# Kernel tuning notes

Hardware: AMD Instinct MI355X
Metric: run time of the kernel (lower is better)

The kernel has to match this reference:

```python
import jax, jax.numpy as jnp
import numpy as np

B, S, D = 32, 512, 512
H, DK, DV, DFF = 8, 64, 64, 2048
TEMP = float(np.sqrt(DK))  # d_k ** 0.5
COS_EPS = 1e-8             # torch.cosine_similarity eps
LN_EPS = 1e-5


def _layernorm(x, g, b):
    mu = jnp.mean(x, axis=-1, keepdims=True)
    var = jnp.var(x, axis=-1, keepdims=True)
    return (x - mu) * jax.lax.rsqrt(var + LN_EPS) * g + b


def setup_inputs() -> dict:
    key = jax.random.key(0)
    ks = jax.random.split(key, 12)
    s = 0.02
    return {
        "x": jax.random.normal(ks[0], (B, S, D), dtype=jnp.float32),
        "w_q": jax.random.normal(ks[1], (D, H * DK), dtype=jnp.float32) * s,
        "w_k": jax.random.normal(ks[2], (D, H * DK), dtype=jnp.float32) * s,
        "w_v": jax.random.normal(ks[3], (D, H * DV), dtype=jnp.float32) * s,
        "w_o": jax.random.normal(ks[4], (H * DV, D), dtype=jnp.float32) * s,
        "w_ff1": jax.random.normal(ks[5], (D, DFF), dtype=jnp.float32) * s,
        "b_ff1": jnp.zeros((DFF,), dtype=jnp.float32),
        "w_ff2": jax.random.normal(ks[6], (DFF, D), dtype=jnp.float32) * s,
        "b_ff2": jnp.zeros((D,), dtype=jnp.float32),
        "g1": jnp.ones((D,), dtype=jnp.float32),
        "b1": jnp.zeros((D,), dtype=jnp.float32),
        "g2": jnp.ones((D,), dtype=jnp.float32),
        "b2": jnp.zeros((D,), dtype=jnp.float32),
    }


def reference(x, w_q, w_k, w_v, w_o, w_ff1, b_ff1, w_ff2, b_ff2, g1, b1, g2, b2):
    b, s, _ = x.shape
    # projections -> [b, h, s, d]
    q = (x @ w_q).reshape(b, s, H, DK).transpose(0, 2, 1, 3)
    k = (x @ w_k).reshape(b, s, H, DK).transpose(0, 2, 1, 3)
    v = (x @ w_v).reshape(b, s, H, DV).transpose(0, 2, 1, 3)
    # cosine-similarity attention: dot(q,k) / max(||q||*||k||, eps) / temperature
    scores = jnp.einsum("bhqd,bhkd->bhqk", q, k)
    nq = jnp.linalg.norm(q, axis=-1)  # [b,h,s]
    nk = jnp.linalg.norm(k, axis=-1)
    denom = jnp.maximum(nq[:, :, :, None] * nk[:, :, None, :], COS_EPS)
    attn = jax.nn.softmax(scores / denom / TEMP, axis=-1)
    out = jnp.einsum("bhqk,bhkd->bhqd", attn, v)  # [b,h,s,dv]
    out = out.transpose(0, 2, 1, 3).reshape(b, s, H * DV) @ w_o
    # residual + LN1
    h1 = _layernorm(x + out, g1, b1)
    # FFN
    ffn = jax.nn.relu(h1 @ w_ff1 + b_ff1) @ w_ff2 + b_ff2
    # residual + LN2
    return _layernorm(h1 + ffn, g2, b2)
```

## Files before the change

### kernel.cpp

```cpp
#include <hip/hip_runtime.h>
#include <cmath>

typedef __bf16 bf16x8 __attribute__((ext_vector_type(8)));
typedef __bf16 bf16x4 __attribute__((ext_vector_type(4)));
typedef float  floatx4 __attribute__((ext_vector_type(4)));

#define LN_EPS 1e-5f
#define INV_TEMP 0.125f

static const int Mrows = 16384;

__device__ __forceinline__ void gload_lds16(const void* g, void* l) {
  __builtin_amdgcn_global_load_lds(
      (const __attribute__((address_space(1))) void*)g,
      (__attribute__((address_space(3))) void*)l, 16, 0, 0);
}

__global__ __launch_bounds__(256) void prep_kernel(const float* __restrict__ x, __bf16* __restrict__ xb,
                                                   const float* __restrict__ wq, const float* __restrict__ wk,
                                                   const float* __restrict__ wv, const float* __restrict__ wo,
                                                   const float* __restrict__ wff1, const float* __restrict__ wff2,
                                                   __bf16* __restrict__ tq, __bf16* __restrict__ tk,
                                                   __bf16* __restrict__ tv, __bf16* __restrict__ to_,
                                                   __bf16* __restrict__ tff1, __bf16* __restrict__ tff2) {
  const int bid = blockIdx.x, tid = threadIdx.x;
  if (bid < 8192) {
    int i = bid * 256 + tid;
    float4 v = ((const float4*)x)[i];
    __bf16* d = xb + i * 4;
    d[0] = (__bf16)v.x; d[1] = (__bf16)v.y; d[2] = (__bf16)v.z; d[3] = (__bf16)v.w;
    return;
  }
  __shared__ __bf16 til[64][72];
  int t = bid - 8192;
  const float* src; __bf16* dst; int R, C, bx, by;
  if (t < 256) {
    int w = t >> 6, tt = t & 63;
    const float* srcs[4] = {wq, wk, wv, wo};
    __bf16* dsts[4] = {tq, tk, tv, to_};
    src = srcs[w]; dst = dsts[w]; R = 512; C = 512; bx = tt & 7; by = tt >> 3;
  } else if (t < 512) {
    int tt = t - 256;
    src = wff1; dst = tff1; R = 512; C = 2048; bx = tt & 31; by = tt >> 5;
  } else {
    int tt = t - 512;
    src = wff2; dst = tff2; R = 2048; C = 512; bx = tt & 7; by = tt >> 3;
  }
  const float* s = src + (size_t)(by * 64) * C + bx * 64;
  int r = tid >> 4, c4 = (tid & 15) * 4;
  for (int p = 0; p < 4; ++p) {
    int rr = r + p * 16;
    float4 v = *(const float4*)(s + (size_t)rr * C + c4);
    til[c4 + 0][rr] = (__bf16)v.x;
    til[c4 + 1][rr] = (__bf16)v.y;
    til[c4 + 2][rr] = (__bf16)v.z;
    til[c4 + 3][rr] = (__bf16)v.w;
  }
  __syncthreads();
  __bf16* d = dst + (size_t)(bx * 64) * R + by * 64;
  int orow = tid >> 3, oc8 = (tid & 7) * 8;
  for (int p = 0; p < 2; ++p) {
    int rr = orow + p * 32;
    *(bf16x8*)(d + (size_t)rr * R + oc8) = *(const bf16x8*)(&til[rr][oc8]);
  }
}

template <int EPI, int NBN, int NDIM, int KDIM>
__global__ __launch_bounds__(256) void gemm_bt(const __bf16* __restrict__ A,
                                               const __bf16* __restrict__ Bt,
                                               __bf16* __restrict__ Cv,
                                               const float* __restrict__ bias,
                                               float* __restrict__ norms,
                                               __bf16* __restrict__ vtg) {
  __shared__ __align__(16) char smem[128 * 144 * 2];
  __bf16* As = (__bf16*)smem;
  __bf16* Bs = (__bf16*)(smem + 16384);
  const int tid = threadIdx.x;
  const int wave = tid >> 6, lane = tid & 63;
  const int l15 = lane & 15, quad = lane >> 4;
  const int id = blockIdx.x;
  const int xcd = id & 7, t = id >> 3;
  const int nblk = t % NBN, mblk = (t / NBN) * 8 + xcd;
  const int m0 = mblk * 128, n0 = nblk * 128;
  const int wrow = (wave >> 1) * 64, wcol = (wave & 1) * 64;
  const int rs = lane >> 3;
  const int swz_st = ((lane & 7) ^ rs) * 8;
  const int s7 = l15 & 7;

  floatx4 zero = {0.f, 0.f, 0.f, 0.f};
  floatx4 acc[4][4];
  for (int i = 0; i < 4; ++i)
    for (int j = 0; j < 4; ++j) acc[i][j] = zero;

  for (int kt = 0; kt < KDIM; kt += 64) {
    __syncthreads();
    for (int c = 0; c < 8; ++c) {
      int g = wave * 8 + c;
      const __bf16* src;
      __bf16* dst;
      if (g < 16) {
        int row = m0 + g * 8 + rs;
        src = A + (size_t)row * KDIM + kt + swz_st;
        dst = As + g * 512;
      } else {
        int g2 = g - 16;
        int row = n0 + g2 * 8 + rs;
        src = Bt + (size_t)row * KDIM + kt + swz_st;
        dst = Bs + g2 * 512;
      }
      gload_lds16(src, dst + lane * 8);
    }
    __syncthreads();
    for (int hh = 0; hh < 2; ++hh) {
      int ko = ((hh * 4 + quad) ^ s7) * 8;
      bf16x8 a[4], b[4];
      for (int i = 0; i < 4; ++i)
        a[i] = *(const bf16x8*)(As + (wrow + i * 16 + l15) * 64 + ko);
      for (int j = 0; j < 4; ++j)
        b[j] = *(const bf16x8*)(Bs + (wcol + j * 16 + l15) * 64 + ko);
      for (int i = 0; i < 4; ++i)
        for (int j = 0; j < 4; ++j)
          acc[i][j] = __builtin_amdgcn_mfma_f32_16x16x32_bf16(a[i], b[j], acc[i][j], 0, 0, 0);
    }
  }

  if (EPI == 4) {
    int head_global = (n0 + wcol) >> 6;
    int kind = head_global >> 3;
    if (kind < 2) {
      int h = head_global & 7;
      for (int i = 0; i < 4; ++i)
        for (int r = 0; r < 4; ++r) {
          float sq = 0.f;
          for (int j = 0; j < 4; ++j) {
            float v = acc[i][j][r];
            sq += v * v;
          }
          for (int m = 1; m < 16; m <<= 1) sq += __shfl_xor(sq, m, 64);
          if (l15 == 0) {
            int arow = m0 + wrow + i * 16 + quad * 4 + r;
            int bb = arow >> 9, ss = arow & 511;
            norms[kind * 131072 + ((bb << 3) + h) * 512 + ss] = rsqrtf(sq);
          }
        }
    } else {
      __syncthreads();
      __bf16* Ct = (__bf16*)smem;
      for (int i = 0; i < 4; ++i)
        for (int j = 0; j < 4; ++j) {
          bf16x4 pk;
          for (int r = 0; r < 4; ++r) pk[r] = (__bf16)acc[i][j][r];
          *(bf16x4*)(Ct + (wcol + j * 16 + l15) * 136 + wrow + i * 16 + quad * 4) = pk;
        }
      __syncthreads();
      int b = mblk >> 2, s0r = (mblk & 3) * 128;
      for (int p = 0; p < 8; ++p) {
        int row = p * 16 + (tid >> 4);
        int c8 = (tid & 15) * 8;
        int colg = n0 + row;
        int h = (colg >> 6) & 7, d = colg & 63;
        *(bf16x8*)(vtg + ((size_t)(((b << 3) + h) * 64 + d)) * 512 + s0r + c8) =
            *(const bf16x8*)(Ct + row * 136 + c8);
      }
      return;
    }
  }

  __syncthreads();
  __bf16* Cs = (__bf16*)smem;
  for (int i = 0; i < 4; ++i)
    for (int j = 0; j < 4; ++j) {
      int coll = wcol + j * 16 + l15;
      float bv = (EPI == 2) ? bias[n0 + coll] : 0.f;
      for (int r = 0; r < 4; ++r) {
        float v = acc[i][j][r];
        if (EPI == 2) {
          v += bv;
          v = v > 0.f ? v : 0.f;
        }
        Cs[(wrow + i * 16 + quad * 4 + r) * 144 + coll] = (__bf16)v;
      }
    }
  __syncthreads();
  for (int p = 0; p < 8; ++p) {
    int row = p * 16 + (tid >> 4);
    int c8 = (tid & 15) * 8;
    *(bf16x8*)(Cv + (size_t)(m0 + row) * NDIM + n0 + c8) =
        *(const bf16x8*)(Cs + row * 144 + c8);
  }
}

__global__ __launch_bounds__(256) void attn_kernel(const __bf16* __restrict__ qkv,
                                                   const __bf16* __restrict__ vtg,
                                                   const float* __restrict__ norms,
                                                   __bf16* __restrict__ out) {
  __shared__ __align__(16) __bf16 Ks[64 * 64];
  __shared__ __align__(16) __bf16 Vs[64 * 64];
  __shared__ __align__(16) __bf16 P2[4][16 * 72];
  const int tid = threadIdx.x, wave = tid >> 6, lane = tid & 63;
  const int l15 = lane & 15, quad = lane >> 4;
  const int bh = blockIdx.x & 255;
  const int qq = blockIdx.x >> 8;
  const int b = bh >> 3, h = bh & 7;
  const int qbase = qq * 128 + wave * 32;
  const int rs = lane >> 3;
  const int swz_st = ((lane & 7) ^ rs) * 8;
  const int s7 = l15 & 7;

  const __bf16* Qb = qkv + (size_t)(b * 512) * 1536 + h * 64;
  const __bf16* Kb = Qb + 512;
  const __bf16* Vtb = vtg + (size_t)bh * 32768;
  const float* nkinv = norms + 131072 + bh * 512;
  const float* nqinv = norms + bh * 512;
  __bf16* Pw = P2[wave];

  bf16x8 aq[2][2];
  float cq[2];
  for (int ch = 0; ch < 2; ++ch) {
    int qrow = qbase + ch * 16;
    aq[ch][0] = *(const bf16x8*)(Qb + (size_t)(qrow + l15) * 1536 + quad * 8);
    aq[ch][1] = *(const bf16x8*)(Qb + (size_t)(qrow + l15) * 1536 + 32 + quad * 8);
    cq[ch] = nqinv[qrow + l15] * INV_TEMP;
  }

  floatx4 zero = {0.f, 0.f, 0.f, 0.f};
  floatx4 o[2][4];
  float lsum[2] = {0.f, 0.f};
  for (int ch = 0; ch < 2; ++ch)
    for (int jd = 0; jd < 4; ++jd) o[ch][jd] = zero;

  for (int kt = 0; kt < 8; ++kt) {
    int s0 = kt * 64;
    __syncthreads();
    for (int c = 0; c < 4; ++c) {
      int g = wave * 4 + c;
      const __bf16* src;
      __bf16* dst;
      if (g < 8) {
        int sk = g * 8 + rs;
        src = Kb + (size_t)(s0 + sk) * 1536 + swz_st;
        dst = Ks + g * 512;
      } else {
        int g2 = g - 8;
        int d = g2 * 8 + rs;
        src = Vtb + (size_t)d * 512 + s0 + swz_st;
        dst = Vs + g2 * 512;
      }
      gload_lds16(src, dst + lane * 8);
    }
    __syncthreads();

    for (int ch = 0; ch < 2; ++ch) {
      floatx4 z[4];
      for (int j = 0; j < 4; ++j) {
        int r64 = (j * 16 + l15) * 64;
        bf16x8 k0 = *(const bf16x8*)(Ks + r64 + ((quad ^ s7) * 8));
        bf16x8 k1 = *(const bf16x8*)(Ks + r64 + (((4 + quad) ^ s7) * 8));
        floatx4 zz = zero;
        zz = __builtin_amdgcn_mfma_f32_16x16x32_bf16(k0, aq[ch][0], zz, 0, 0, 0);
        zz = __builtin_amdgcn_mfma_f32_16x16x32_bf16(k1, aq[ch][1], zz, 0, 0, 0);
        z[j] = zz;
      }
      for (int j = 0; j < 4; ++j) {
        floatx4 nk4 = *(const floatx4*)(nkinv + s0 + j * 16 + quad * 4);
        bf16x4 pk;
        for (int r = 0; r < 4; ++r) {
          float p = __expf(z[j][r] * cq[ch] * nk4[r]);
          lsum[ch] += p;
          pk[r] = (__bf16)p;
        }
        *(bf16x4*)(Pw + l15 * 72 + j * 16 + quad * 4) = pk;
      }
      bf16x8 ap0 = *(const bf16x8*)(Pw + l15 * 72 + quad * 8);
      bf16x8 ap1 = *(const bf16x8*)(Pw + l15 * 72 + 32 + quad * 8);
      for (int jd = 0; jd < 4; ++jd) {
        int r64 = (jd * 16 + l15) * 64;
        bf16x8 v0 = *(const bf16x8*)(Vs + r64 + ((quad ^ s7) * 8));
        bf16x8 v1 = *(const bf16x8*)(Vs + r64 + (((4 + quad) ^ s7) * 8));
        o[ch][jd] = __builtin_amdgcn_mfma_f32_16x16x32_bf16(v0, ap0, o[ch][jd], 0, 0, 0);
        o[ch][jd] = __builtin_amdgcn_mfma_f32_16x16x32_bf16(v1, ap1, o[ch][jd], 0, 0, 0);
      }
    }
  }

  for (int ch = 0; ch < 2; ++ch) {
    float s = lsum[ch];
    s += __shfl_xor(s, 16, 64);
    s += __shfl_xor(s, 32, 64);
    float inv = __builtin_amdgcn_rcpf(s);
    int q = qbase + ch * 16 + l15;
    __bf16* op = out + (size_t)(b * 512 + q) * 512 + h * 64;
    for (int jd = 0; jd < 4; ++jd) {
      bf16x4 pk;
      for (int r = 0; r < 4; ++r) pk[r] = (__bf16)(o[ch][jd][r] * inv);
      *(bf16x4*)(op + jd * 16 + quad * 4) = pk;
    }
  }
}

template <bool X1BF, bool WF, bool WB>
__global__ __launch_bounds__(256) void resid_ln(const float* __restrict__ X1f,
                                                const __bf16* __restrict__ X1b,
                                                const __bf16* __restrict__ X2,
                                                const float* __restrict__ bias,
                                                const float* __restrict__ g,
                                                const float* __restrict__ be,
                                                float* __restrict__ outf,
                                                __bf16* __restrict__ outb) {
  int row = blockIdx.x * 4 + (threadIdx.x >> 6);
  int lane = threadIdx.x & 63;
  float v[8];
  bf16x8 b8 = *(const bf16x8*)(X2 + (size_t)row * 512 + lane * 8);
  if (X1BF) {
    bf16x8 a = *(const bf16x8*)(X1b + (size_t)row * 512 + lane * 8);
    for (int i = 0; i < 8; ++i) v[i] = (float)a[i] + (float)b8[i];
  } else {
    const float4* r1 = (const float4*)(X1f + (size_t)row * 512);
    float4 a0 = r1[lane * 2], a1 = r1[lane * 2 + 1];
    v[0] = a0.x; v[1] = a0.y; v[2] = a0.z; v[3] = a0.w;
    v[4] = a1.x; v[5] = a1.y; v[6] = a1.z; v[7] = a1.w;
    for (int i = 0; i < 8; ++i) v[i] += (float)b8[i];
  }
  if (bias) {
    const float* bp = bias + lane * 8;
    for (int i = 0; i < 8; ++i) v[i] += bp[i];
  }
  float s = 0.f, sq = 0.f;
  for (int i = 0; i < 8; ++i) {
    s += v[i];
    sq += v[i] * v[i];
  }
  for (int m = 1; m < 64; m <<= 1) {
    s += __shfl_xor(s, m, 64);
    sq += __shfl_xor(sq, m, 64);
  }
  float mean = s * (1.f / 512.f);
  float var = sq * (1.f / 512.f) - mean * mean;
  float rstd = rsqrtf(var + LN_EPS);
  const float* gp = g + lane * 8;
  const float* bp2 = be + lane * 8;
  float o[8];
  for (int i = 0; i < 8; ++i) o[i] = (v[i] - mean) * rstd * gp[i] + bp2[i];
  if (WF) {
    float4 w0 = {o[0], o[1], o[2], o[3]}, w1 = {o[4], o[5], o[6], o[7]};
    ((float4*)(outf + (size_t)row * 512))[lane * 2] = w0;
    ((float4*)(outf + (size_t)row * 512))[lane * 2 + 1] = w1;
  }
  if (WB) {
    __bf16 tmp[8];
    for (int i = 0; i < 8; ++i) tmp[i] = (__bf16)o[i];
    *(bf16x8*)(outb + (size_t)row * 512 + lane * 8) = *(bf16x8*)tmp;
  }
}

extern "C" void kernel_launch(void* const* d_in, const int* in_sizes, int n_in,
                              void* d_out, int out_size, void* d_ws, size_t ws_size,
                              hipStream_t stream) {
  const float* x     = (const float*)d_in[0];
  const float* w_q   = (const float*)d_in[1];
  const float* w_k   = (const float*)d_in[2];
  const float* w_v   = (const float*)d_in[3];
  const float* w_o   = (const float*)d_in[4];
  const float* w_ff1 = (const float*)d_in[5];
  const float* b_ff1 = (const float*)d_in[6];
  const float* w_ff2 = (const float*)d_in[7];
  const float* b_ff2 = (const float*)d_in[8];
  const float* g1    = (const float*)d_in[9];
  const float* b1    = (const float*)d_in[10];
  const float* g2    = (const float*)d_in[11];
  const float* b2    = (const float*)d_in[12];
  float* out = (float*)d_out;

  char* ws = (char*)d_ws;
  size_t off = 0;
  auto alloc = [&](size_t bytes) -> void* {
    void* p = ws + off;
    off += (bytes + 255) & ~(size_t)255;
    return p;
  };
  __bf16* xb     = (__bf16*)alloc((size_t)Mrows * 512 * 2);
  __bf16* wt_qkv = (__bf16*)alloc((size_t)1536 * 512 * 2);
  __bf16* wt_o   = (__bf16*)alloc((size_t)512 * 512 * 2);
  __bf16* wt_ff1 = (__bf16*)alloc((size_t)2048 * 512 * 2);
  __bf16* wt_ff2 = (__bf16*)alloc((size_t)512 * 2048 * 2);
  __bf16* qkv    = (__bf16*)alloc((size_t)Mrows * 1536 * 2);
  float*  norms  = (float*)alloc((size_t)262144 * 4);
  __bf16* attn   = (__bf16*)alloc((size_t)Mrows * 512 * 2);
  __bf16* projb  = (__bf16*)alloc((size_t)Mrows * 512 * 2);
  __bf16* h1b    = (__bf16*)alloc((size_t)Mrows * 512 * 2);
  __bf16* mid    = (__bf16*)alloc((size_t)Mrows * 2048 * 2);
  __bf16* vtg    = mid;
  __bf16* f2o    = attn;

  prep_kernel<<<8960, 256, 0, stream>>>(x, xb, w_q, w_k, w_v, w_o, w_ff1, w_ff2,
                                        wt_qkv, wt_qkv + 512 * 512, wt_qkv + 2 * 512 * 512,
                                        wt_o, wt_ff1, wt_ff2);

  gemm_bt<4, 12, 1536, 512><<<dim3(12 * 128), 256, 0, stream>>>(xb, wt_qkv, qkv, nullptr,
                                                                norms, vtg);
  attn_kernel<<<dim3(1024), 256, 0, stream>>>(qkv, vtg, norms, attn);
  gemm_bt<0, 4, 512, 512><<<dim3(4 * 128), 256, 0, stream>>>(attn, wt_o, projb, nullptr,
                                                             nullptr, nullptr);
  resid_ln<false, false, true><<<4096, 256, 0, stream>>>(x, nullptr, projb, nullptr,
                                                         g1, b1, nullptr, h1b);
  gemm_bt<2, 16, 2048, 512><<<dim3(16 * 128), 256, 0, stream>>>(h1b, wt_ff1, mid, b_ff1,
                                                                nullptr, nullptr);
  gemm_bt<0, 4, 512, 2048><<<dim3(4 * 128), 256, 0, stream>>>(mid, wt_ff2, f2o, nullptr,
                                                              nullptr, nullptr);
  resid_ln<true, true, false><<<4096, 256, 0, stream>>>(nullptr, h1b, f2o, b_ff2,
                                                        g2, b2, out, nullptr);
}
```

Before: 329.9 us.

## Use 256x256-tile pipelined GEMM for FFN layers with split-K for FFN2

Adds a 512-thread GEMM kernel with 256x256 output tiles. It double-buffers 64-wide K slices in LDS through direct global-to-LDS loads and interleaves the MFMA phases with the staging of the next slice. The FFN1 and FFN2 GEMMs now use this kernel, and FFN2 is split into two K halves whose bf16 partial results are summed in the final residual+LayerNorm kernel. The aim is more data reuse per tile and a better fill of the CUs for the narrow FFN2 output. In exchange it uses 128KB of LDS per block, rounds the split-K partials to bf16, and writes the second partial past the attn buffer into the adjacent allocation.

```diff
diff --git a/kernel.cpp b/kernel.cpp
--- a/kernel.cpp
+++ b/kernel.cpp
@@ -190,6 +190,167 @@
   }
 }
 
+template <int EPI, int NBN, int NDIM, int KDIM, int NKS>
+__global__ __launch_bounds__(512, 2) void gemm256(const __bf16* __restrict__ A,
+                                                  const __bf16* __restrict__ Bt,
+                                                  __bf16* __restrict__ Cv,
+                                                  const float* __restrict__ bias) {
+  __shared__ __align__(16) char smem[131072];
+  const int tid = threadIdx.x;
+  const int wave = tid >> 6, lane = tid & 63;
+  const int l15 = lane & 15, quad = lane >> 4;
+  const int wm = wave >> 2, wn = wave & 3;
+  const int s7 = l15 & 7;
+  const int rs = lane >> 3, slot = lane & 7;
+  const int swz = (slot ^ rs) * 8;
+
+  constexpr int NBM = Mrows / 256;
+  constexpr int NBLK = NBM * NBN * NKS;
+  constexpr int KS = KDIM / NKS;
+  constexpr int NT = KS / 64;
+
+  int id = blockIdx.x;
+  int t = (id & 7) * (NBLK >> 3) + (id >> 3);
+  const int ks = t / (NBM * NBN);
+  t -= ks * (NBM * NBN);
+  const int nblk = t % NBN, mblk = t / NBN;
+  const int m0 = mblk * 256, n0 = nblk * 256;
+  const __bf16* Ab = A + (size_t)ks * KS;
+  const __bf16* Bb = Bt + (size_t)ks * KS;
+  __bf16* Cw = Cv + (size_t)ks * Mrows * NDIM;
+  (void)bias;
+
+  const __bf16* sb[4][2];
+  int ldo[4][2];
+#pragma unroll
+  for (int s = 0; s < 4; ++s)
+#pragma unroll
+    for (int j = 0; j < 2; ++j) {
+      int chunk;
+      if (s < 2) {
+        int c = (wave & 3) * 4 + s * 2 + j;
+        if (wave < 4) chunk = (c < 8) ? c : c + 8;
+        else          chunk = 32 + ((c >> 2) * 8 + (c & 3));
+      } else if (s == 2) {
+        int c = 2 * wave + j;
+        chunk = (c < 8) ? c + 8 : c + 16;
+      } else {
+        int c = 2 * wave + j;
+        chunk = 32 + ((c >> 2) * 8 + 4 + (c & 3));
+      }
+      int isB = chunk >= 32 ? 1 : 0;
+      int cc = chunk - isB * 32;
+      int row = cc * 8 + rs;
+      sb[s][j] = (isB ? (Bb + (size_t)(n0 + row) * KDIM)
+                      : (Ab + (size_t)(m0 + row) * KDIM)) + swz;
+      ldo[s][j] = isB * 32768 + cc * 1024 + lane * 16;
+    }
+
+  floatx4 zero = {0.f, 0.f, 0.f, 0.f};
+  floatx4 acc[8][4];
+#pragma unroll
+  for (int i = 0; i < 8; ++i)
+#pragma unroll
+    for (int j = 0; j < 4; ++j) acc[i][j] = zero;
+
+#define STAGE256(s, ktel, bufb)                                              \
+  {                                                                          \
+    gload_lds16(sb[s][0] + (ktel), smem + (bufb) * 65536 + ldo[s][0]);       \
+    gload_lds16(sb[s][1] + (ktel), smem + (bufb) * 65536 + ldo[s][1]);       \
+  }
+
+#define PHASE256(q, ia, jb, bufb, DOSTAGE, ktel)                                   \
+  {                                                                                \
+    const __bf16* Abuf = (const __bf16*)(smem + (bufb) * 65536);                   \
+    const __bf16* Bbuf = Abuf + 16384;                                             \
+    bf16x8 af[4][2], bfr[2][2];                                                    \
+    _Pragma("unroll") for (int i = 0; i < 4; ++i) {                                \
+      int row = wm * 128 + (ia) * 64 + i * 16 + l15;                               \
+      af[i][0] = *(const bf16x8*)(Abuf + row * 64 + ((quad ^ s7) * 8));            \
+      af[i][1] = *(const bf16x8*)(Abuf + row * 64 + (((4 + quad) ^ s7) * 8));      \
+    }                                                                              \
+    _Pragma("unroll") for (int j = 0; j < 2; ++j) {                                \
+      int row = wn * 64 + (jb) * 32 + j * 16 + l15;                                \
+      bfr[j][0] = *(const bf16x8*)(Bbuf + row * 64 + ((quad ^ s7) * 8));           \
+      bfr[j][1] = *(const bf16x8*)(Bbuf + row * 64 + (((4 + quad) ^ s7) * 8));     \
+    }                                                                              \
+    if (DOSTAGE) STAGE256(q, ktel, (bufb) ^ 1);                                    \
+    __builtin_amdgcn_s_barrier();                                                  \
+    asm volatile("s_waitcnt lgkmcnt(0)" ::: "memory");                             \
+    __builtin_amdgcn_s_setprio(1);                                                 \
+    _Pragma("unroll") for (int i = 0; i < 4; ++i)                                  \
+      _Pragma("unroll") for (int j = 0; j < 2; ++j) {                              \
+        acc[(ia) * 4 + i][(jb) * 2 + j] = __builtin_amdgcn_mfma_f32_16x16x32_bf16( \
+            af[i][0], bfr[j][0], acc[(ia) * 4 + i][(jb) * 2 + j], 0, 0, 0);        \
+        acc[(ia) * 4 + i][(jb) * 2 + j] = __builtin_amdgcn_mfma_f32_16x16x32_bf16( \
+            af[i][1], bfr[j][1], acc[(ia) * 4 + i][(jb) * 2 + j], 0, 0, 0);        \
+      }                                                                            \
+    __builtin_amdgcn_s_setprio(0);                                                 \
+    asm volatile("s_waitcnt vmcnt(4)" ::: "memory");                               \
+    __builtin_amdgcn_s_barrier();                                                  \
+  }
+
+#pragma unroll
+  for (int s = 0; s < 4; ++s) STAGE256(s, 0, 0);
+  asm volatile("s_waitcnt vmcnt(0)" ::: "memory");
+  __builtin_amdgcn_s_barrier();
+
+  for (int t2 = 0; t2 < NT - 1; ++t2) {
+    int b = t2 & 1;
+    int k1 = (t2 + 1) * 64;
+    PHASE256(0, 0, 0, b, 1, k1);
+    PHASE256(1, 1, 0, b, 1, k1);
+    PHASE256(2, 1, 1, b, 1, k1);
+    PHASE256(3, 0, 1, b, 1, k1);
+  }
+  asm volatile("s_waitcnt vmcnt(0)" ::: "memory");
+  __builtin_amdgcn_s_barrier();
+  {
+    const int b = (NT - 1) & 1;
+    PHASE256(0, 0, 0, b, 0, 0);
+    PHASE256(1, 1, 0, b, 0, 0);
+    PHASE256(2, 1, 1, b, 0, 0);
+    PHASE256(3, 0, 1, b, 0, 0);
+  }
+
+  const int PADC = 264;
+  __bf16* Cs = (__bf16*)smem;
+  float bv[4];
+  if (EPI == 2) {
+#pragma unroll
+    for (int j = 0; j < 4; ++j) bv[j] = bias[n0 + wn * 64 + j * 16 + l15];
+  }
+#pragma unroll
+  for (int hh = 0; hh < 2; ++hh) {
+    __builtin_amdgcn_s_barrier();
+    if (wm == hh) {
+#pragma unroll
+      for (int i = 0; i < 8; ++i)
+#pragma unroll
+        for (int j = 0; j < 4; ++j)
+#pragma unroll
+          for (int r = 0; r < 4; ++r) {
+            float v = acc[i][j][r];
+            if (EPI == 2) {
+              v += bv[j];
+              v = v > 0.f ? v : 0.f;
+            }
+            Cs[(i * 16 + quad * 4 + r) * PADC + wn * 64 + j * 16 + l15] = (__bf16)v;
+          }
+    }
+    __builtin_amdgcn_s_barrier();
+#pragma unroll
+    for (int p = 0; p < 8; ++p) {
+      int rowl = p * 16 + (tid >> 5);
+      int c8 = (tid & 31) * 8;
+      *(bf16x8*)(Cw + (size_t)(m0 + hh * 128 + rowl) * NDIM + n0 + c8) =
+          *(const bf16x8*)(Cs + rowl * PADC + c8);
+    }
+  }
+#undef STAGE256
+#undef PHASE256
+}
+
 __global__ __launch_bounds__(256) void attn_kernel(const __bf16* __restrict__ qkv,
                                                    const __bf16* __restrict__ vtg,
                                                    const float* __restrict__ norms,
@@ -298,10 +459,11 @@
   }
 }
 
-template <bool X1BF, bool WF, bool WB>
+template <bool X1BF, bool WF, bool WB, bool DUAL>
 __global__ __launch_bounds__(256) void resid_ln(const float* __restrict__ X1f,
                                                 const __bf16* __restrict__ X1b,
                                                 const __bf16* __restrict__ X2,
+                                                const __bf16* __restrict__ X2b,
                                                 const float* __restrict__ bias,
                                                 const float* __restrict__ g,
                                                 const float* __restrict__ be,
@@ -320,6 +482,10 @@
     v[0] = a0.x; v[1] = a0.y; v[2] = a0.z; v[3] = a0.w;
     v[4] = a1.x; v[5] = a1.y; v[6] = a1.z; v[7] = a1.w;
     for (int i = 0; i < 8; ++i) v[i] += (float)b8[i];
+  }
+  if (DUAL) {
+    bf16x8 c8 = *(const bf16x8*)(X2b + (size_t)row * 512 + lane * 8);
+    for (int i = 0; i < 8; ++i) v[i] += (float)c8[i];
   }
   if (bias) {
     const float* bp = bias + lane * 8;
@@ -401,12 +567,11 @@
   attn_kernel<<<dim3(1024), 256, 0, stream>>>(qkv, vtg, norms, attn);
   gemm_bt<0, 4, 512, 512><<<dim3(4 * 128), 256, 0, stream>>>(attn, wt_o, projb, nullptr,
                                                              nullptr, nullptr);
-  resid_ln<false, false, true><<<4096, 256, 0, stream>>>(x, nullptr, projb, nullptr,
-                                                         g1, b1, nullptr, h1b);
-  gemm_bt<2, 16, 2048, 512><<<dim3(16 * 128), 256, 0, stream>>>(h1b, wt_ff1, mid, b_ff1,
-                                                                nullptr, nullptr);
-  gemm_bt<0, 4, 512, 2048><<<dim3(4 * 128), 256, 0, stream>>>(mid, wt_ff2, f2o, nullptr,
-                                                              nullptr, nullptr);
-  resid_ln<true, true, false><<<4096, 256, 0, stream>>>(nullptr, h1b, f2o, b_ff2,
-                                                        g2, b2, out, nullptr);
-}
+  resid_ln<false, false, true, false><<<4096, 256, 0, stream>>>(x, nullptr, projb, nullptr,
+                                                                nullptr, g1, b1, nullptr, h1b);
+  gemm256<2, 8, 2048, 512, 1><<<dim3(512), 512, 0, stream>>>(h1b, wt_ff1, mid, b_ff1);
+  gemm256<0, 2, 512, 2048, 2><<<dim3(256), 512, 0, stream>>>(mid, wt_ff2, f2o, nullptr);
+  resid_ln<true, true, false, true><<<4096, 256, 0, stream>>>(nullptr, h1b, f2o,
+                                                              f2o + (size_t)Mrows * 512,
+                                                              b_ff2, g2, b2, out, nullptr);
+}
```

Measured after the change: 320.9 us. 2.7% less time.

## Use 256x256 multistage-pipelined GEMM with split-K reduced inside LayerNorm

Applied to the files above, without the earlier changes.

Replaces the 128x128 single-buffered GEMM with a 512-thread, 256x256-tile kernel. Each K=32 slice is staged through a 4-slot LDS ring with global_load_lds prefetch three slices ahead, raw barriers with vmcnt waits, and MFMA priority boosting. The two N=512 GEMMs (output projection and FF2) now run as 2-way split-K, writing partial results to separate buffers. The residual-LayerNorm kernel sums the two partials, so no extra reduction kernel is needed. This is meant to raise arithmetic intensity and overlap loads with compute. The cost is 128KB of LDS per block, fewer blocks for small GEMMs, and extra partial-buffer traffic.

```diff
diff --git a/kernel.cpp b/kernel.cpp
--- a/kernel.cpp
+++ b/kernel.cpp
@@ -65,128 +65,178 @@
   }
 }
 
-template <int EPI, int NBN, int NDIM, int KDIM>
-__global__ __launch_bounds__(256) void gemm_bt(const __bf16* __restrict__ A,
-                                               const __bf16* __restrict__ Bt,
-                                               __bf16* __restrict__ Cv,
-                                               const float* __restrict__ bias,
-                                               float* __restrict__ norms,
-                                               __bf16* __restrict__ vtg) {
-  __shared__ __align__(16) char smem[128 * 144 * 2];
-  __bf16* As = (__bf16*)smem;
-  __bf16* Bs = (__bf16*)(smem + 16384);
+template <int EPI, int NBN, int NDIM, int KDIM, int NKS>
+__global__ __launch_bounds__(512, 2) void gemm256(const __bf16* __restrict__ A,
+                                                  const __bf16* __restrict__ Bt,
+                                                  __bf16* __restrict__ Cv,
+                                                  const float* __restrict__ bias,
+                                                  float* __restrict__ norms,
+                                                  __bf16* __restrict__ vtg) {
+  __shared__ __align__(16) char smem[131072];
   const int tid = threadIdx.x;
   const int wave = tid >> 6, lane = tid & 63;
   const int l15 = lane & 15, quad = lane >> 4;
-  const int id = blockIdx.x;
-  const int xcd = id & 7, t = id >> 3;
-  const int nblk = t % NBN, mblk = (t / NBN) * 8 + xcd;
-  const int m0 = mblk * 128, n0 = nblk * 128;
-  const int wrow = (wave >> 1) * 64, wcol = (wave & 1) * 64;
-  const int rs = lane >> 3;
-  const int swz_st = ((lane & 7) ^ rs) * 8;
-  const int s7 = l15 & 7;
+  const int wm = wave >> 2, wn = wave & 3;
+
+  constexpr int NBM = Mrows / 256;
+  constexpr int NBLK = NBM * NBN * NKS;
+  constexpr int KS = KDIM / NKS;
+  constexpr int NTH = KS / 32;
+
+  int id = blockIdx.x;
+  int t = (id & 7) * (NBLK >> 3) + (id >> 3);
+  const int ks = t / (NBM * NBN);
+  t -= ks * (NBM * NBN);
+  const int nblk = t % NBN, mblk = t / NBN;
+  const int m0 = mblk * 256, n0 = nblk * 256;
+  const __bf16* Ab = A + (size_t)ks * KS;
+  const __bf16* Bb = Bt + (size_t)ks * KS;
+  __bf16* Cw = Cv + (size_t)ks * Mrows * NDIM;
+  (void)bias;
+
+  const int wq = wave & 3, isB = wave >> 2;
+  const int l3 = lane >> 3, sl7 = lane & 7;
+  const int slog = sl7 ^ l3;
+  const int wbit = slog & 1, kseg = slog >> 1;
+  const int rl = l3 * 2 + wbit;
+  const __bf16* sbase = (isB ? Bb + (size_t)(n0 + wq * 64 + rl) * KDIM
+                             : Ab + (size_t)(m0 + wq * 64 + rl) * KDIM) + kseg * 8;
+  const int ldob = isB * 16384 + wq * 4096 + lane * 16;
+
+  const int rsw = (l15 >> 1) * 128 + ((((quad << 1) | (l15 & 1)) ^ (l15 >> 1)) * 16);
+  const int wmBase = wm * 8192;
+  const int wnBase = wn * 4096;
 
   floatx4 zero = {0.f, 0.f, 0.f, 0.f};
-  floatx4 acc[4][4];
-  for (int i = 0; i < 4; ++i)
+  floatx4 acc[8][4];
+#pragma unroll
+  for (int i = 0; i < 8; ++i)
+#pragma unroll
     for (int j = 0; j < 4; ++j) acc[i][j] = zero;
 
-  for (int kt = 0; kt < KDIM; kt += 64) {
-    __syncthreads();
-    for (int c = 0; c < 8; ++c) {
-      int g = wave * 8 + c;
-      const __bf16* src;
-      __bf16* dst;
-      if (g < 16) {
-        int row = m0 + g * 8 + rs;
-        src = A + (size_t)row * KDIM + kt + swz_st;
-        dst = As + g * 512;
-      } else {
-        int g2 = g - 16;
-        int row = n0 + g2 * 8 + rs;
-        src = Bt + (size_t)row * KDIM + kt + swz_st;
-        dst = Bs + g2 * 512;
-      }
-      gload_lds16(src, dst + lane * 8);
-    }
-    __syncthreads();
-    for (int hh = 0; hh < 2; ++hh) {
-      int ko = ((hh * 4 + quad) ^ s7) * 8;
-      bf16x8 a[4], b[4];
-      for (int i = 0; i < 4; ++i)
-        a[i] = *(const bf16x8*)(As + (wrow + i * 16 + l15) * 64 + ko);
-      for (int j = 0; j < 4; ++j)
-        b[j] = *(const bf16x8*)(Bs + (wcol + j * 16 + l15) * 64 + ko);
-      for (int i = 0; i < 4; ++i)
-        for (int j = 0; j < 4; ++j)
-          acc[i][j] = __builtin_amdgcn_mfma_f32_16x16x32_bf16(a[i], b[j], acc[i][j], 0, 0, 0);
-    }
-  }
+#define STAGEH(h)                                                            \
+  {                                                                          \
+    _Pragma("unroll") for (int j = 0; j < 4; ++j)                            \
+        gload_lds16(sbase + (size_t)j * (16 * KDIM) + (h) * 32,              \
+                    smem + ((h) & 3) * 32768 + ldob + j * 1024);             \
+  }
+
+#define PHASE(h, DOSTAGE, VM)                                                \
+  {                                                                          \
+    asm volatile("s_waitcnt vmcnt(" #VM ")" ::: "memory");                   \
+    __builtin_amdgcn_s_barrier();                                            \
+    const char* slotp = smem + ((h) & 3) * 32768;                            \
+    bf16x8 aF[8], bF[4];                                                     \
+    _Pragma("unroll") for (int i = 0; i < 8; ++i)                            \
+      aF[i] = *(const bf16x8*)(slotp + wmBase + i * 1024 + rsw);             \
+    _Pragma("unroll") for (int j = 0; j < 4; ++j)                            \
+      bF[j] = *(const bf16x8*)(slotp + 16384 + wnBase + j * 1024 + rsw);     \
+    if (DOSTAGE) STAGEH((h) + 3);                                            \
+    __builtin_amdgcn_s_setprio(1);                                           \
+    _Pragma("unroll") for (int i = 0; i < 8; ++i)                            \
+      _Pragma("unroll") for (int j = 0; j < 4; ++j)                          \
+        acc[i][j] = __builtin_amdgcn_mfma_f32_16x16x32_bf16(aF[i], bF[j],    \
+                                                            acc[i][j], 0, 0, 0); \
+    __builtin_amdgcn_s_setprio(0);                                           \
+  }
+
+  STAGEH(0); STAGEH(1); STAGEH(2);
+
+  for (int h = 0; h <= NTH - 4; ++h) PHASE(h, 1, 8);
+  PHASE(NTH - 3, 0, 8);
+  PHASE(NTH - 2, 0, 4);
+  PHASE(NTH - 1, 0, 0);
+
+#undef STAGEH
+#undef PHASE
 
   if (EPI == 4) {
-    int head_global = (n0 + wcol) >> 6;
+    int head_global = (n0 + wn * 64) >> 6;
     int kind = head_global >> 3;
     if (kind < 2) {
       int h = head_global & 7;
-      for (int i = 0; i < 4; ++i)
+#pragma unroll
+      for (int ii = 0; ii < 8; ++ii)
+#pragma unroll
         for (int r = 0; r < 4; ++r) {
           float sq = 0.f;
-          for (int j = 0; j < 4; ++j) {
-            float v = acc[i][j][r];
+#pragma unroll
+          for (int jj = 0; jj < 4; ++jj) {
+            float v = acc[ii][jj][r];
             sq += v * v;
           }
           for (int m = 1; m < 16; m <<= 1) sq += __shfl_xor(sq, m, 64);
           if (l15 == 0) {
-            int arow = m0 + wrow + i * 16 + quad * 4 + r;
+            int arow = m0 + wm * 128 + ii * 16 + quad * 4 + r;
             int bb = arow >> 9, ss = arow & 511;
             norms[kind * 131072 + ((bb << 3) + h) * 512 + ss] = rsqrtf(sq);
           }
         }
     } else {
-      __syncthreads();
+      const int PADT = 136;
       __bf16* Ct = (__bf16*)smem;
-      for (int i = 0; i < 4; ++i)
-        for (int j = 0; j < 4; ++j) {
-          bf16x4 pk;
-          for (int r = 0; r < 4; ++r) pk[r] = (__bf16)acc[i][j][r];
-          *(bf16x4*)(Ct + (wcol + j * 16 + l15) * 136 + wrow + i * 16 + quad * 4) = pk;
+      int bb = m0 >> 9, s0r = m0 & 511;
+#pragma unroll
+      for (int hh = 0; hh < 2; ++hh) {
+        __builtin_amdgcn_s_barrier();
+        if (wm == hh) {
+#pragma unroll
+          for (int ii = 0; ii < 8; ++ii)
+#pragma unroll
+            for (int jj = 0; jj < 4; ++jj) {
+              bf16x4 pk;
+#pragma unroll
+              for (int r = 0; r < 4; ++r) pk[r] = (__bf16)acc[ii][jj][r];
+              *(bf16x4*)(Ct + (wn * 64 + jj * 16 + l15) * PADT + ii * 16 + quad * 4) = pk;
+            }
         }
-      __syncthreads();
-      int b = mblk >> 2, s0r = (mblk & 3) * 128;
-      for (int p = 0; p < 8; ++p) {
-        int row = p * 16 + (tid >> 4);
-        int c8 = (tid & 15) * 8;
-        int colg = n0 + row;
-        int h = (colg >> 6) & 7, d = colg & 63;
-        *(bf16x8*)(vtg + ((size_t)(((b << 3) + h) * 64 + d)) * 512 + s0r + c8) =
-            *(const bf16x8*)(Ct + row * 136 + c8);
+        __builtin_amdgcn_s_barrier();
+#pragma unroll
+        for (int p = 0; p < 8; ++p) {
+          int c = p * 32 + (tid >> 4);
+          int s8 = (tid & 15) * 8;
+          int h = ((n0 + c) >> 6) & 7, d = c & 63;
+          *(bf16x8*)(vtg + ((size_t)(((bb << 3) + h) * 64 + d)) * 512 + s0r + hh * 128 + s8) =
+              *(const bf16x8*)(Ct + c * PADT + s8);
+        }
       }
       return;
     }
   }
 
-  __syncthreads();
+  const int PADC = 264;
   __bf16* Cs = (__bf16*)smem;
-  for (int i = 0; i < 4; ++i)
-    for (int j = 0; j < 4; ++j) {
-      int coll = wcol + j * 16 + l15;
-      float bv = (EPI == 2) ? bias[n0 + coll] : 0.f;
-      for (int r = 0; r < 4; ++r) {
-        float v = acc[i][j][r];
-        if (EPI == 2) {
-          v += bv;
-          v = v > 0.f ? v : 0.f;
-        }
-        Cs[(wrow + i * 16 + quad * 4 + r) * 144 + coll] = (__bf16)v;
-      }
-    }
-  __syncthreads();
-  for (int p = 0; p < 8; ++p) {
-    int row = p * 16 + (tid >> 4);
-    int c8 = (tid & 15) * 8;
-    *(bf16x8*)(Cv + (size_t)(m0 + row) * NDIM + n0 + c8) =
-        *(const bf16x8*)(Cs + row * 144 + c8);
+  float bv[4];
+  if (EPI == 2) {
+#pragma unroll
+    for (int j = 0; j < 4; ++j) bv[j] = bias[n0 + wn * 64 + j * 16 + l15];
+  }
+#pragma unroll
+  for (int hh = 0; hh < 2; ++hh) {
+    __builtin_amdgcn_s_barrier();
+    if (wm == hh) {
+#pragma unroll
+      for (int i = 0; i < 8; ++i)
+#pragma unroll
+        for (int j = 0; j < 4; ++j)
+#pragma unroll
+          for (int r = 0; r < 4; ++r) {
+            float v = acc[i][j][r];
+            if (EPI == 2) {
+              v += bv[j];
+              v = v > 0.f ? v : 0.f;
+            }
+            Cs[(i * 16 + quad * 4 + r) * PADC + wn * 64 + j * 16 + l15] = (__bf16)v;
+          }
+    }
+    __builtin_amdgcn_s_barrier();
+#pragma unroll
+    for (int p = 0; p < 8; ++p) {
+      int rowl = p * 16 + (tid >> 5);
+      int c8 = (tid & 31) * 8;
+      *(bf16x8*)(Cw + (size_t)(m0 + hh * 128 + rowl) * NDIM + n0 + c8) =
+          *(const bf16x8*)(Cs + rowl * PADC + c8);
+    }
   }
 }
 
@@ -298,10 +348,11 @@
   }
 }
 
-template <bool X1BF, bool WF, bool WB>
+template <bool X1BF, bool WF, bool WB, bool DUAL>
 __global__ __launch_bounds__(256) void resid_ln(const float* __restrict__ X1f,
                                                 const __bf16* __restrict__ X1b,
                                                 const __bf16* __restrict__ X2,
+                                                const __bf16* __restrict__ X2b,
                                                 const float* __restrict__ bias,
                                                 const float* __restrict__ g,
                                                 const float* __restrict__ be,
@@ -320,6 +371,10 @@
     v[0] = a0.x; v[1] = a0.y; v[2] = a0.z; v[3] = a0.w;
     v[4] = a1.x; v[5] = a1.y; v[6] = a1.z; v[7] = a1.w;
     for (int i = 0; i < 8; ++i) v[i] += (float)b8[i];
+  }
+  if (DUAL) {
+    bf16x8 c8 = *(const bf16x8*)(X2b + (size_t)row * 512 + lane * 8);
+    for (int i = 0; i < 8; ++i) v[i] += (float)c8[i];
   }
   if (bias) {
     const float* bp = bias + lane * 8;
@@ -390,23 +445,26 @@
   __bf16* h1b    = (__bf16*)alloc((size_t)Mrows * 512 * 2);
   __bf16* mid    = (__bf16*)alloc((size_t)Mrows * 2048 * 2);
   __bf16* vtg    = mid;
+  __bf16* wo_p   = mid;
   __bf16* f2o    = attn;
 
   prep_kernel<<<8960, 256, 0, stream>>>(x, xb, w_q, w_k, w_v, w_o, w_ff1, w_ff2,
                                         wt_qkv, wt_qkv + 512 * 512, wt_qkv + 2 * 512 * 512,
                                         wt_o, wt_ff1, wt_ff2);
 
-  gemm_bt<4, 12, 1536, 512><<<dim3(12 * 128), 256, 0, stream>>>(xb, wt_qkv, qkv, nullptr,
-                                                                norms, vtg);
+  gemm256<4, 6, 1536, 512, 1><<<dim3(384), 512, 0, stream>>>(xb, wt_qkv, qkv, nullptr,
+                                                             norms, vtg);
   attn_kernel<<<dim3(1024), 256, 0, stream>>>(qkv, vtg, norms, attn);
-  gemm_bt<0, 4, 512, 512><<<dim3(4 * 128), 256, 0, stream>>>(attn, wt_o, projb, nullptr,
+  gemm256<0, 2, 512, 512, 2><<<dim3(256), 512, 0, stream>>>(attn, wt_o, wo_p, nullptr,
+                                                            nullptr, nullptr);
+  resid_ln<false, false, true, true><<<4096, 256, 0, stream>>>(x, nullptr, wo_p,
+                                                               wo_p + (size_t)Mrows * 512,
+                                                               nullptr, g1, b1, nullptr, h1b);
+  gemm256<2, 8, 2048, 512, 1><<<dim3(512), 512, 0, stream>>>(h1b, wt_ff1, mid, b_ff1,
                                                              nullptr, nullptr);
-  resid_ln<false, false, true><<<4096, 256, 0, stream>>>(x, nullptr, projb, nullptr,
-                                                         g1, b1, nullptr, h1b);
-  gemm_bt<2, 16, 2048, 512><<<dim3(16 * 128), 256, 0, stream>>>(h1b, wt_ff1, mid, b_ff1,
-                                                                nullptr, nullptr);
-  gemm_bt<0, 4, 512, 2048><<<dim3(4 * 128), 256, 0, stream>>>(mid, wt_ff2, f2o, nullptr,
-                                                              nullptr, nullptr);
-  resid_ln<true, true, false><<<4096, 256, 0, stream>>>(nullptr, h1b, f2o, b_ff2,
-                                                        g2, b2, out, nullptr);
-}
+  gemm256<0, 2, 512, 2048, 2><<<dim3(256), 512, 0, stream>>>(mid, wt_ff2, f2o, nullptr,
+                                                             nullptr, nullptr);
+  resid_ln<true, true, false, true><<<4096, 256, 0, stream>>>(nullptr, h1b, f2o,
+                                                              f2o + (size_t)Mrows * 512,
+                                                              b_ff2, g2, b2, out, nullptr);
+}
```

After: 333.7 us. No clear change (+1.2%).
